# Optimization experiments

Hardware: AMD Instinct MI355X
Metric: run time of the kernel (lower is better)

## Reference

```python
import jax, jax.numpy as jnp
import numpy as np
from jax import lax

V, D, H, HR = 32000, 512, 1024, 2
T_SRC, T_TGT, T_REF, B, NREF = 128, 128, 32, 64, 4


def _gru_scan(x_emb, lengths, h0, Wih, Whh, bih, bhh):
    """Masked GRU over padded [T,B,D]; equivalent to torch pack->GRU->unpack.
    Returns (outputs [T,B,h] zeroed past lengths, final hidden [B,h])."""
    T = x_emb.shape[0]
    xW = jnp.einsum('tbd,gd->tbg', x_emb, Wih) + bih  # [T,B,3h] input-gate preacts

    def step(h, inp):
        xw, t = inp
        hw = h @ Whh.T + bhh
        xr, xz, xn = jnp.split(xw, 3, axis=-1)
        hr, hz, hn = jnp.split(hw, 3, axis=-1)
        r = jax.nn.sigmoid(xr + hr)
        z = jax.nn.sigmoid(xz + hz)
        n = jnp.tanh(xn + r * hn)
        h_new = (1.0 - z) * n + z * h
        m = (t < lengths)[:, None]
        h_next = jnp.where(m, h_new, h)   # freeze hidden past length (packing)
        out = jnp.where(m, h_new, 0.0)    # unpack pads with zeros
        return h_next, out

    hT, outs = lax.scan(step, h0, (xW, jnp.arange(T)))
    return outs, hT


def setup_inputs() -> dict:
    key = jax.random.key(0)
    ks = jax.random.split(key, 32)

    def u(k, shape, fan):
        lim = 1.0 / np.sqrt(fan)
        return jax.random.uniform(k, shape, jnp.float32, -lim, lim)

    inp = {}
    inp['tgt'] = jax.random.randint(ks[0], (T_TGT, B), 0, V)
    inp['tgt_lengths'] = jax.random.randint(ks[1], (B,), 1, T_TGT + 1)
    inp['src'] = jax.random.randint(ks[2], (T_SRC, B), 0, V)
    inp['src_lengths'] = jax.random.randint(ks[3], (B,), 1, T_SRC + 1)
    inp['ref_ids'] = jax.random.randint(ks[4], (NREF, T_REF, B), 0, V)
    inp['ref_lengths'] = jax.random.randint(ks[5], (NREF, B), 1, T_REF + 1)
    inp['emb'] = jax.random.normal(ks[6], (V, D), jnp.float32) * 0.02
    inp['src_Wih'] = u(ks[7], (3 * H, D), H)
    inp['src_Whh'] = u(ks[8], (3 * H, H), H)
    inp['src_bih'] = u(ks[9], (3 * H,), H)
    inp['src_bhh'] = u(ks[10], (3 * H,), H)
    inp['tgt_Wih'] = u(ks[11], (3 * H, D), H)
    inp['tgt_Whh'] = u(ks[12], (3 * H, H), H)
    inp['tgt_bih'] = u(ks[13], (3 * H,), H)
    inp['tgt_bhh'] = u(ks[14], (3 * H,), H)
    inp['ref_Wih'] = u(ks[15], (3 * HR, D), HR)
    inp['ref_Whh'] = u(ks[16], (3 * HR, HR), HR)
    inp['ref_bih'] = u(ks[17], (3 * HR,), HR)
    inp['ref_bhh'] = u(ks[18], (3 * HR,), HR)
    inp['p1_W'] = u(ks[19], (64, H), H)
    inp['p1_b'] = u(ks[20], (64,), H)
    inp['p2_W'] = u(ks[21], (2, 64), 64)
    inp['p2_b'] = u(ks[22], (2,), 64)
    return inp


def reference(tgt, tgt_lengths, src, src_lengths, ref_ids, ref_lengths, emb,
              src_Wih, src_Whh, src_bih, src_bhh,
              tgt_Wih, tgt_Whh, tgt_bih, tgt_bhh,
              ref_Wih, ref_Whh, ref_bih, ref_bhh,
              p1_W, p1_b, p2_W, p2_b):
    # --- src encoder ---
    src_emb = emb[src]  # [T_SRC,B,D]
    h0 = jnp.zeros((src.shape[1], src_Whh.shape[1]), emb.dtype)
    _, src_hT = _gru_scan(src_emb, src_lengths, h0, src_Wih, src_Whh, src_bih, src_bhh)

    # --- ref encoders: original loops in Python over the ref list with
    # per-ref sort/pack/tiny-GRU; here vectorized with vmap over NREF.
    # (Output is computed, as torch eager does, but does not feed logits.)
    ref_emb = emb[ref_ids]  # [NREF,T_REF,B,D]
    h0r = jnp.zeros((ref_ids.shape[2], ref_Whh.shape[1]), emb.dtype)
    ref_context, ref_hidden = jax.vmap(
        lambda e, l: _gru_scan(e, l, h0r, ref_Wih, ref_Whh, ref_bih, ref_bhh)
    )(ref_emb, ref_lengths)
    del ref_context, ref_hidden

    # --- tgt decoder initialized from src final hidden ---
    tgt_emb = emb[tgt]
    _, tgt_hT = _gru_scan(tgt_emb, tgt_lengths, src_hT, tgt_Wih, tgt_Whh, tgt_bih, tgt_bhh)

    # --- projection head (dropout = identity in eval) ---
    logits = jnp.tanh(tgt_hT @ p1_W.T + p1_b) @ p2_W.T + p2_b  # [B,2]
    return logits
```

## Files before the change

kernel.cpp:

```cpp
#include <hip/hip_runtime.h>
#include <stdint.h>

typedef short short8 __attribute__((ext_vector_type(8)));
typedef float f32x4 __attribute__((ext_vector_type(4)));
typedef float f32x2 __attribute__((ext_vector_type(2)));
typedef unsigned long long u64;

#define TSEQ   128
#define BATCH  64
#define DIM    512
#define HID    1024
#define G3     3072
#define MROWS  (TSEQ * BATCH)
#define NB     32
#define HB     32

__device__ __forceinline__ unsigned short f2bf(float f) {
  union { float f; unsigned u; } v; v.f = f;
  unsigned u = v.u;
  return (unsigned short)((u + 0x7FFFu + ((u >> 16) & 1u)) >> 16);
}

__device__ __forceinline__ short8 pack8(f32x4 a, f32x4 b) {
  short8 r;
  r[0] = (short)f2bf(a.x); r[1] = (short)f2bf(a.y);
  r[2] = (short)f2bf(a.z); r[3] = (short)f2bf(a.w);
  r[4] = (short)f2bf(b.x); r[5] = (short)f2bf(b.y);
  r[6] = (short)f2bf(b.z); r[7] = (short)f2bf(b.w);
  return r;
}

__device__ __forceinline__ u64 packbf4(float a, float b, float c, float d) {
  return (u64)f2bf(a) | ((u64)f2bf(b) << 16) | ((u64)f2bf(c) << 32) | ((u64)f2bf(d) << 48);
}

__device__ __forceinline__ float sigm(float x) { return 1.0f / (1.0f + __expf(-x)); }
__device__ __forceinline__ float tanh_fast(float x) { return 2.0f / (1.0f + __expf(-2.0f * x)) - 1.0f; }

__global__ __launch_bounds__(256) void prep_kernel(
    const int* __restrict__ ids, const float* __restrict__ emb,
    const float* __restrict__ wih, unsigned short* __restrict__ X,
    unsigned short* __restrict__ Wb, unsigned int* bars)
{
  int row = blockIdx.x;
  int tid = threadIdx.x;
  const float* srcp;
  unsigned short* dst;
  if (row < MROWS) {
    srcp = emb + (long)ids[row] * DIM;
    dst  = X + (long)row * DIM;
  } else {
    int wr = row - MROWS;
    srcp = wih + (long)wr * DIM;
    dst  = Wb + (long)wr * DIM;
  }
  int d = tid * 2;
  f32x2 v = *(const f32x2*)(srcp + d);
  unsigned pk = (unsigned)f2bf(v.x) | ((unsigned)f2bf(v.y) << 16);
  *(unsigned*)(dst + d) = pk;
  if (bars != nullptr && row == 0) ((f32x4*)bars)[tid] = (f32x4){};
}

#define BM 128
#define BN 128
#define BK 32

__global__ __launch_bounds__(256) void xw_gemm(
    const unsigned short* __restrict__ X,
    const unsigned short* __restrict__ W,
    const float* __restrict__ bih,
    float* __restrict__ out)
{
  __shared__ unsigned short As[BM * BK];
  __shared__ unsigned short Bs[BN * BK];
  int tid = threadIdx.x;
  int w = tid >> 6, l = tid & 63;
  int m0 = blockIdx.y * BM;
  int n0 = blockIdx.x * BN;
  int wr = w >> 1, wc = w & 1;

  int sr = tid >> 2, skq = tid & 3;
  int sr2 = sr + 64;
  int sgk  = (skq - (sr  >> 1)) & 3;
  int sgk2 = (skq - (sr2 >> 1)) & 3;
  const unsigned short* gA0 = X + (long)(m0 + sr ) * DIM + sgk  * 8;
  const unsigned short* gA1 = X + (long)(m0 + sr2) * DIM + sgk2 * 8;
  const unsigned short* gB0 = W + (long)(n0 + sr ) * DIM + sgk  * 8;
  const unsigned short* gB1 = W + (long)(n0 + sr2) * DIM + sgk2 * 8;
  unsigned short* lA0 = As + sr  * BK + skq * 8;
  unsigned short* lA1 = As + sr2 * BK + skq * 8;
  unsigned short* lB0 = Bs + sr  * BK + skq * 8;
  unsigned short* lB1 = Bs + sr2 * BK + skq * 8;

  f32x4 acc[4][4];
  #pragma unroll
  for (int mt = 0; mt < 4; ++mt)
    #pragma unroll
    for (int nt = 0; nt < 4; ++nt) acc[mt][nt] = (f32x4){};

  short8 va0 = *(const short8*)(gA0);
  short8 va1 = *(const short8*)(gA1);
  short8 vb0 = *(const short8*)(gB0);
  short8 vb1 = *(const short8*)(gB1);

  int fr = l & 15, fk = l >> 4;
  for (int kt = 0; kt < DIM / BK; ++kt) {
    __syncthreads();
    *(short8*)lA0 = va0; *(short8*)lA1 = va1;
    *(short8*)lB0 = vb0; *(short8*)lB1 = vb1;
    __syncthreads();
    if (kt + 1 < DIM / BK) {
      int ko = (kt + 1) * BK;
      va0 = *(const short8*)(gA0 + ko);
      va1 = *(const short8*)(gA1 + ko);
      vb0 = *(const short8*)(gB0 + ko);
      vb1 = *(const short8*)(gB1 + ko);
    }
    short8 af[4], bf[4];
    #pragma unroll
    for (int mt = 0; mt < 4; ++mt) {
      int r = wr * 64 + mt * 16 + fr;
      int slot = ((r >> 1) + fk) & 3;
      af[mt] = *(const short8*)(As + r * BK + slot * 8);
    }
    #pragma unroll
    for (int nt = 0; nt < 4; ++nt) {
      int r = wc * 64 + nt * 16 + fr;
      int slot = ((r >> 1) + fk) & 3;
      bf[nt] = *(const short8*)(Bs + r * BK + slot * 8);
    }
    #pragma unroll
    for (int mt = 0; mt < 4; ++mt)
      #pragma unroll
      for (int nt = 0; nt < 4; ++nt)
        acc[mt][nt] = __builtin_amdgcn_mfma_f32_16x16x32_bf16(af[mt], bf[nt], acc[mt][nt], 0, 0, 0);
  }

  #pragma unroll
  for (int nt = 0; nt < 4; ++nt) {
    int n = n0 + wc * 64 + nt * 16 + fr;
    float bias = bih[n];
    #pragma unroll
    for (int mt = 0; mt < 4; ++mt) {
      int mbase = m0 + wr * 64 + mt * 16 + fk * 4;
      #pragma unroll
      for (int r = 0; r < 4; ++r)
        out[(long)(mbase + r) * G3 + n] = acc[mt][nt][r] + bias;
    }
  }
}

#define MF(a, b, c) __builtin_amdgcn_mfma_f32_16x16x32_bf16(a, b, c, 0, 0, 0)

#define ISSUE(ss, kk) do { \
  asm volatile("global_load_dwordx4 %0, %1, off offset:%2 sc0" \
               : "=v"(bv[ss][0]) : "v"(ad0), "i"((kk) * 64) : "memory"); \
  asm volatile("global_load_dwordx4 %0, %1, off offset:%2 sc0" \
               : "=v"(bv[ss][1]) : "v"(ad1), "i"((kk) * 64) : "memory"); \
  asm volatile("global_load_dwordx4 %0, %1, off offset:%2 sc0" \
               : "=v"(bv[ss][2]) : "v"(ad2), "i"((kk) * 64) : "memory"); \
  asm volatile("global_load_dwordx4 %0, %1, off offset:%2 sc0" \
               : "=v"(bv[ss][3]) : "v"(ad3), "i"((kk) * 64) : "memory"); \
} while (0)

#define MF6(kk, ss, nt) \
  acc[0][nt] = MF(areg[0][kk], bv[ss][nt], acc[0][nt]); \
  acc[1][nt] = MF(areg[1][kk], bv[ss][nt], acc[1][nt]); \
  acc[2][nt] = MF(areg[2][kk], bv[ss][nt], acc[2][nt]); \
  acc[3][nt] = MF(areg[3][kk], bv[ss][nt], acc[3][nt]); \
  acc[4][nt] = MF(areg[4][kk], bv[ss][nt], acc[4][nt]); \
  acc[5][nt] = MF(areg[5][kk], bv[ss][nt], acc[5][nt]);

#define CONS(kk, ss, wn) do { \
  asm volatile("s_waitcnt vmcnt(" #wn ")" ::: "memory"); \
  __builtin_amdgcn_sched_barrier(0); \
  MF6(kk, ss, 0) MF6(kk, ss, 1) MF6(kk, ss, 2) MF6(kk, ss, 3) \
} while (0)

#define CONSI(kk, ss, wn, nk) do { CONS(kk, ss, wn); ISSUE(ss, nk); } while (0)

#define BARRIER_ARRIVE(tgtv) do { \
  asm volatile("s_waitcnt vmcnt(0)" ::: "memory"); \
  __syncthreads(); \
  if (tid == 0) { \
    unsigned fv_ = (unsigned)(tgtv); \
    uint64_t fa_ = (uint64_t)(bar + (blockIdx.x << 4)); \
    asm volatile("global_store_dword %0, %1, off sc0 sc1" :: "v"(fa_), "v"(fv_) : "memory"); \
  } \
} while (0)

#define BARRIER_WAIT(tgtv) do { \
  if (tid < NB) { \
    unsigned v_; \
    uint64_t pa_ = (uint64_t)(bar + (tid << 4)); \
    do { \
      asm volatile("global_load_dword %0, %1, off sc0 sc1" : "=v"(v_) : "v"(pa_) : "memory"); \
      asm volatile("s_waitcnt vmcnt(0)" ::: "memory"); \
    } while (__any(v_ < (unsigned)(tgtv))); \
  } \
  __syncthreads(); \
  asm volatile("buffer_inv sc1" ::: "memory"); \
} while (0)

__global__ __launch_bounds__(256, 1) void gru_kernel(
    const float* __restrict__ Whh, const float* __restrict__ bhh,
    const float* __restrict__ xw, const int* __restrict__ lengths,
    u64* __restrict__ hbf,
    float* __restrict__ hf32,
    unsigned int* __restrict__ bar, int T, int initzero)
{
  const int tid = threadIdx.x;
  const int w = tid >> 6, l = tid & 63;
  const int fr = l & 15, fk = l >> 4;
  const int U0 = blockIdx.x * HB;

  short8 areg[6][8];
  #pragma unroll
  for (int mt = 0; mt < 6; ++mt) {
    const int m = mt * 16 + fr;
    const int gate = m >> 5, u = m & 31;
    const float* wp = Whh + (size_t)(gate * HID + U0 + u) * HID + w * 256 + fk * 8;
    #pragma unroll
    for (int ksl = 0; ksl < 8; ++ksl) {
      f32x4 a0 = *(const f32x4*)(wp + ksl * 32);
      f32x4 a1 = *(const f32x4*)(wp + ksl * 32 + 4);
      areg[mt][ksl] = pack8(a0, a1);
    }
  }

  const int gb = l;
  const int j0 = w * 8;
  const size_t hoff = (size_t)gb * (HID / 4) + (size_t)(U0 + j0) / 4;
  const int len_b = lengths[gb];

  float h[8];
  #pragma unroll
  for (int j = 0; j < 8; ++j)
    h[j] = initzero ? 0.0f : hf32[(size_t)gb * HID + U0 + j0 + j];

  __shared__ float red2[4][64][100];
  __shared__ float bb[3][32];
  if (tid < 96) bb[tid >> 5][tid & 31] = bhh[(tid >> 5) * HID + U0 + (tid & 31)];

  f32x4 xrv[2], xzv[2], xnv[2];
  #define LOAD_XW(tt) do { \
    const float* xp_ = xw + ((size_t)(tt) * BATCH + gb) * G3 + U0 + j0; \
    xrv[0] = *(const f32x4*)(xp_);            xrv[1] = *(const f32x4*)(xp_ + 4); \
    xzv[0] = *(const f32x4*)(xp_ + HID);      xzv[1] = *(const f32x4*)(xp_ + HID + 4); \
    xnv[0] = *(const f32x4*)(xp_ + 2 * HID);  xnv[1] = *(const f32x4*)(xp_ + 2 * HID + 4); \
  } while (0)

  {
    union { u64 q[2]; f32x4 v4; } pk;
    pk.q[0] = packbf4(h[0], h[1], h[2], h[3]);
    pk.q[1] = packbf4(h[4], h[5], h[6], h[7]);
    uint64_t hw = (uint64_t)(hbf + hoff);
    asm volatile("global_store_dwordx4 %0, %1, off sc0 sc1" :: "v"(hw), "v"(pk.v4) : "memory");
    BARRIER_ARRIVE(1);
    LOAD_XW(0);
    BARRIER_WAIT(1);
  }

  for (int t = 0; t < T; ++t) {
    asm volatile("s_waitcnt vmcnt(0)" ::: "memory");

    const char* hbase = (const char*)hbf + (size_t)(t & 1) * (BATCH * (HID / 4) * 8);
    uint64_t ad0 = (uint64_t)(hbase + (size_t)(fr) * 2048 + w * 512 + fk * 16);
    uint64_t ad1 = ad0 + 16 * 2048;
    uint64_t ad2 = ad0 + 32 * 2048;
    uint64_t ad3 = ad0 + 48 * 2048;

    f32x4 acc[6][4];
    #pragma unroll
    for (int mt = 0; mt < 6; ++mt)
      #pragma unroll
      for (int nt = 0; nt < 4; ++nt) acc[mt][nt] = (f32x4){};

    short8 bv[6][4];
    ISSUE(0, 0); ISSUE(1, 1); ISSUE(2, 2); ISSUE(3, 3); ISSUE(4, 4); ISSUE(5, 5);
    CONSI(0, 0, 20, 6);
    CONSI(1, 1, 20, 7);
    CONS(2, 2, 20);
    CONS(3, 3, 16);
    CONS(4, 4, 12);
    CONS(5, 5, 8);
    CONS(6, 0, 4);
    CONS(7, 1, 0);

    #pragma unroll
    for (int mt = 0; mt < 6; ++mt)
      #pragma unroll
      for (int nt = 0; nt < 4; ++nt)
        *(f32x4*)&red2[w][nt * 16 + fr][mt * 16 + fk * 4] = acc[mt][nt];
    __syncthreads();

    #define RD4(s, row) (*(const f32x4*)&red2[s][gb][row])
    f32x4 sr_[2], sz_[2], sn_[2];
    #pragma unroll
    for (int hh = 0; hh < 2; ++hh) {
      const int rbase = j0 + hh * 4;
      sr_[hh] = RD4(0, rbase)      + RD4(1, rbase)      + RD4(2, rbase)      + RD4(3, rbase)      + *(const f32x4*)&bb[0][rbase];
      sz_[hh] = RD4(0, 32 + rbase) + RD4(1, 32 + rbase) + RD4(2, 32 + rbase) + RD4(3, 32 + rbase) + *(const f32x4*)&bb[1][rbase];
      sn_[hh] = RD4(0, 64 + rbase) + RD4(1, 64 + rbase) + RD4(2, 64 + rbase) + RD4(3, 64 + rbase) + *(const f32x4*)&bb[2][rbase];
    }

    const int upd = (t < len_b);
    #pragma unroll
    for (int j = 0; j < 8; ++j) {
      float rr = sigm(xrv[j >> 2][j & 3] + sr_[j >> 2][j & 3]);
      float zz = sigm(xzv[j >> 2][j & 3] + sz_[j >> 2][j & 3]);
      float nn = tanh_fast(xnv[j >> 2][j & 3] + rr * sn_[j >> 2][j & 3]);
      float cc = (1.0f - zz) * nn + zz * h[j];
      h[j] = upd ? cc : h[j];
    }

    if (t + 1 < T) {
      union { u64 q[2]; f32x4 v4; } pk;
      pk.q[0] = packbf4(h[0], h[1], h[2], h[3]);
      pk.q[1] = packbf4(h[4], h[5], h[6], h[7]);
      uint64_t hw = (uint64_t)((char*)hbf + (size_t)((t + 1) & 1) * (BATCH * (HID / 4) * 8) + hoff * 8);
      asm volatile("global_store_dwordx4 %0, %1, off sc0 sc1" :: "v"(hw), "v"(pk.v4) : "memory");
      BARRIER_ARRIVE(t + 2);
      LOAD_XW(t + 1);
      BARRIER_WAIT(t + 2);
    }
  }

  #pragma unroll
  for (int j = 0; j < 8; ++j)
    hf32[(size_t)gb * HID + U0 + j0 + j] = h[j];
}

__global__ __launch_bounds__(256) void head_kernel(
    const float* __restrict__ hf32, const float* __restrict__ p1W,
    const float* __restrict__ p1b, const float* __restrict__ p2W,
    const float* __restrict__ p2b, float* __restrict__ outp)
{
  int b = blockIdx.x;
  int tid = threadIdx.x;
  __shared__ float hrow[HID];
  __shared__ float red[4][64];
  __shared__ float s1[64];
  for (int d = tid; d < HID; d += 256) hrow[d] = hf32[(long)b * HID + d];
  __syncthreads();
  int j = tid & 63, q = tid >> 6;
  const float* wrow = p1W + (long)j * HID + q * 256;
  float s = 0.0f;
  for (int k = 0; k < 256; ++k) s += hrow[q * 256 + k] * wrow[k];
  red[q][j] = s;
  __syncthreads();
  if (tid < 64) {
    float v = red[0][tid] + red[1][tid] + red[2][tid] + red[3][tid] + p1b[tid];
    s1[tid] = tanh_fast(v);
  }
  __syncthreads();
  if (tid < 2) {
    float a = p2b[tid];
    for (int k = 0; k < 64; ++k) a += s1[k] * p2W[tid * 64 + k];
    outp[b * 2 + tid] = a;
  }
}

extern "C" void kernel_launch(void* const* d_in, const int* in_sizes, int n_in,
                              void* d_out, int out_size, void* d_ws, size_t ws_size,
                              hipStream_t stream) {
  const int*   tgt_ids = (const int*)d_in[0];
  const int*   tgt_len = (const int*)d_in[1];
  const int*   src_ids = (const int*)d_in[2];
  const int*   src_len = (const int*)d_in[3];
  const float* emb  = (const float*)d_in[6];
  const float* sWih = (const float*)d_in[7];
  const float* sWhh = (const float*)d_in[8];
  const float* sbih = (const float*)d_in[9];
  const float* sbhh = (const float*)d_in[10];
  const float* tWih = (const float*)d_in[11];
  const float* tWhh = (const float*)d_in[12];
  const float* tbih = (const float*)d_in[13];
  const float* tbhh = (const float*)d_in[14];
  const float* p1W  = (const float*)d_in[19];
  const float* p1b  = (const float*)d_in[20];
  const float* p2W  = (const float*)d_in[21];
  const float* p2b  = (const float*)d_in[22];

  char* ws = (char*)d_ws;
  size_t off = 0;
  float* xw = (float*)(ws + off);                   off += (size_t)MROWS * G3 * 4;
  unsigned short* X  = (unsigned short*)(ws + off); off += (size_t)MROWS * DIM * 2;
  unsigned short* Wb = (unsigned short*)(ws + off); off += (size_t)G3 * DIM * 2;
  u64* hbf = (u64*)(ws + off);                      off += 2ull * BATCH * (HID / 4) * 8;
  float* hf32 = (float*)(ws + off);                 off += (size_t)BATCH * HID * 4;
  unsigned int* bars = (unsigned int*)(ws + off);   off += 4096;
  if (ws_size < off) return;

  const int PREP_BLOCKS = MROWS + G3;

  prep_kernel<<<PREP_BLOCKS, 256, 0, stream>>>(src_ids, emb, sWih, X, Wb, bars);
  xw_gemm<<<dim3(G3 / BN, MROWS / BM), 256, 0, stream>>>(X, Wb, sbih, xw);
  gru_kernel<<<NB, 256, 0, stream>>>(sWhh, sbhh, xw, src_len, hbf, hf32, bars, TSEQ, 1);
  prep_kernel<<<PREP_BLOCKS, 256, 0, stream>>>(tgt_ids, emb, tWih, X, Wb, nullptr);
  xw_gemm<<<dim3(G3 / BN, MROWS / BM), 256, 0, stream>>>(X, Wb, tbih, xw);
  gru_kernel<<<NB, 256, 0, stream>>>(tWhh, tbhh, xw, tgt_len, hbf, hf32, bars + 512, TSEQ, 0);
  head_kernel<<<BATCH, 256, 0, stream>>>(hf32, p1W, p1b, p2W, p2b, (float*)d_out);
}
```

Baseline: 2.316 ms.

## Co-locate GRU blocks on a single XCC to use cheaper L2-scope barriers

The GRU kernel now launches 256 blocks. Each block reads its XCC id and claims a rank with an atomic counter. The first XCC to collect 32 blocks keeps them and the other blocks exit. A probe round checks that hidden-state stores with sc0-only visibility are seen by all 32 ranks; if so, the recurrent loop uses sc0-only stores and loads for hidden state and barrier flags and skips buffer_inv, which avoids cross-XCC coherence traffic on every timestep. This adds extra blocks, a startup handshake and a larger barrier workspace, and it relies on same-XCC L2 coherence; a fallback keeps the old scopes when the probe fails.

Measured after the change: 3.976 ms. 1.72x slower.

```diff
diff --git a/kernel.cpp b/kernel.cpp
--- a/kernel.cpp
+++ b/kernel.cpp
@@ -13,7 +13,13 @@
 #define G3     3072
 #define MROWS  (TSEQ * BATCH)
 #define NB     32
+#define GRID_GRU 256
 #define HB     32
+
+#define FLAGS_OFF 0
+#define PROBE_OFF 4096
+#define OK_OFF    8192
+#define CTL_OFF   12288
 
 __device__ __forceinline__ unsigned short f2bf(float f) {
   union { float f; unsigned u; } v; v.f = f;
@@ -58,7 +64,10 @@
   f32x2 v = *(const f32x2*)(srcp + d);
   unsigned pk = (unsigned)f2bf(v.x) | ((unsigned)f2bf(v.y) << 16);
   *(unsigned*)(dst + d) = pk;
-  if (bars != nullptr && row == 0) ((f32x4*)bars)[tid] = (f32x4){};
+  if (bars != nullptr && row == 0) {
+    #pragma unroll
+    for (int k = 0; k < 8; ++k) ((f32x4*)bars)[k * 256 + tid] = (f32x4){};
+  }
 }
 
 #define BM 128
@@ -179,86 +188,70 @@
 
 #define CONSI(kk, ss, wn, nk) do { CONS(kk, ss, wn); ISSUE(ss, nk); } while (0)
 
-#define BARRIER_ARRIVE(tgtv) do { \
-  asm volatile("s_waitcnt vmcnt(0)" ::: "memory"); \
-  __syncthreads(); \
-  if (tid == 0) { \
-    unsigned fv_ = (unsigned)(tgtv); \
-    uint64_t fa_ = (uint64_t)(bar + (blockIdx.x << 4)); \
-    asm volatile("global_store_dword %0, %1, off sc0 sc1" :: "v"(fa_), "v"(fv_) : "memory"); \
-  } \
-} while (0)
-
-#define BARRIER_WAIT(tgtv) do { \
-  if (tid < NB) { \
-    unsigned v_; \
-    uint64_t pa_ = (uint64_t)(bar + (tid << 4)); \
-    do { \
-      asm volatile("global_load_dword %0, %1, off sc0 sc1" : "=v"(v_) : "v"(pa_) : "memory"); \
-      asm volatile("s_waitcnt vmcnt(0)" ::: "memory"); \
-    } while (__any(v_ < (unsigned)(tgtv))); \
-  } \
-  __syncthreads(); \
-  asm volatile("buffer_inv sc1" ::: "memory"); \
-} while (0)
-
-__global__ __launch_bounds__(256, 1) void gru_kernel(
-    const float* __restrict__ Whh, const float* __restrict__ bhh,
-    const float* __restrict__ xw, const int* __restrict__ lengths,
-    u64* __restrict__ hbf,
-    float* __restrict__ hf32,
-    unsigned int* __restrict__ bar, int T, int initzero)
-{
-  const int tid = threadIdx.x;
-  const int w = tid >> 6, l = tid & 63;
-  const int fr = l & 15, fk = l >> 4;
-  const int U0 = blockIdx.x * HB;
-
-  short8 areg[6][8];
-  #pragma unroll
-  for (int mt = 0; mt < 6; ++mt) {
-    const int m = mt * 16 + fr;
-    const int gate = m >> 5, u = m & 31;
-    const float* wp = Whh + (size_t)(gate * HID + U0 + u) * HID + w * 256 + fk * 8;
-    #pragma unroll
-    for (int ksl = 0; ksl < 8; ++ksl) {
-      f32x4 a0 = *(const f32x4*)(wp + ksl * 32);
-      f32x4 a1 = *(const f32x4*)(wp + ksl * 32 + 4);
-      areg[mt][ksl] = pack8(a0, a1);
-    }
-  }
-
-  const int gb = l;
-  const int j0 = w * 8;
-  const size_t hoff = (size_t)gb * (HID / 4) + (size_t)(U0 + j0) / 4;
-  const int len_b = lengths[gb];
-
-  float h[8];
-  #pragma unroll
-  for (int j = 0; j < 8; ++j)
-    h[j] = initzero ? 0.0f : hf32[(size_t)gb * HID + U0 + j0 + j];
-
-  __shared__ float red2[4][64][100];
-  __shared__ float bb[3][32];
-  if (tid < 96) bb[tid >> 5][tid & 31] = bhh[(tid >> 5) * HID + U0 + (tid & 31)];
-
-  f32x4 xrv[2], xzv[2], xnv[2];
-  #define LOAD_XW(tt) do { \
+#define LOAD_XW(tt) do { \
     const float* xp_ = xw + ((size_t)(tt) * BATCH + gb) * G3 + U0 + j0; \
     xrv[0] = *(const f32x4*)(xp_);            xrv[1] = *(const f32x4*)(xp_ + 4); \
     xzv[0] = *(const f32x4*)(xp_ + HID);      xzv[1] = *(const f32x4*)(xp_ + HID + 4); \
     xnv[0] = *(const f32x4*)(xp_ + 2 * HID);  xnv[1] = *(const f32x4*)(xp_ + 2 * HID + 4); \
   } while (0)
 
+template<bool FAST>
+__device__ __forceinline__ void st_h16(uint64_t a, f32x4 v) {
+  if constexpr (FAST)
+    asm volatile("global_store_dwordx4 %0, %1, off sc0" :: "v"(a), "v"(v) : "memory");
+  else
+    asm volatile("global_store_dwordx4 %0, %1, off sc0 sc1" :: "v"(a), "v"(v) : "memory");
+}
+
+template<bool FAST>
+__device__ __forceinline__ void bar_arrive(unsigned* flags, unsigned rank, unsigned gen, int tid) {
+  asm volatile("s_waitcnt vmcnt(0)" ::: "memory");
+  __syncthreads();
+  if (tid == 0) {
+    uint64_t fa = (uint64_t)(flags + (rank << 4));
+    if constexpr (FAST)
+      asm volatile("global_store_dword %0, %1, off sc0" :: "v"(fa), "v"(gen) : "memory");
+    else
+      asm volatile("global_store_dword %0, %1, off sc0 sc1" :: "v"(fa), "v"(gen) : "memory");
+  }
+}
+
+template<bool FAST, bool INV>
+__device__ __forceinline__ void bar_wait(unsigned* flags, unsigned gen, int tid) {
+  if (tid < NB) {
+    unsigned v;
+    uint64_t pa = (uint64_t)(flags + (tid << 4));
+    do {
+      if constexpr (FAST)
+        asm volatile("global_load_dword %0, %1, off sc0" : "=v"(v) : "v"(pa) : "memory");
+      else
+        asm volatile("global_load_dword %0, %1, off sc0 sc1" : "=v"(v) : "v"(pa) : "memory");
+      asm volatile("s_waitcnt vmcnt(0)" ::: "memory");
+    } while (__any(v < gen));
+  }
+  __syncthreads();
+  if constexpr (INV) asm volatile("buffer_inv sc1" ::: "memory");
+}
+
+template<bool FAST>
+__device__ __forceinline__ void run_gru(
+    const short8 (&areg)[6][8], float (&h)[8],
+    const float* __restrict__ xw, u64* __restrict__ hbf,
+    unsigned* __restrict__ flags, float* __restrict__ hf32,
+    float (*red2)[64][100], float (*bb)[32],
+    int tid, int w, int fr, int fk, int gb, int j0,
+    unsigned rank, int U0, size_t hoff, int len_b, int T)
+{
+  f32x4 xrv[2], xzv[2], xnv[2];
+
   {
     union { u64 q[2]; f32x4 v4; } pk;
     pk.q[0] = packbf4(h[0], h[1], h[2], h[3]);
     pk.q[1] = packbf4(h[4], h[5], h[6], h[7]);
-    uint64_t hw = (uint64_t)(hbf + hoff);
-    asm volatile("global_store_dwordx4 %0, %1, off sc0 sc1" :: "v"(hw), "v"(pk.v4) : "memory");
-    BARRIER_ARRIVE(1);
+    st_h16<FAST>((uint64_t)(hbf + hoff), pk.v4);
+    bar_arrive<FAST>(flags, rank, 2u, tid);
     LOAD_XW(0);
-    BARRIER_WAIT(1);
+    bar_wait<FAST, !FAST>(flags, 2u, tid);
   }
 
   for (int t = 0; t < T; ++t) {
@@ -319,16 +312,119 @@
       pk.q[0] = packbf4(h[0], h[1], h[2], h[3]);
       pk.q[1] = packbf4(h[4], h[5], h[6], h[7]);
       uint64_t hw = (uint64_t)((char*)hbf + (size_t)((t + 1) & 1) * (BATCH * (HID / 4) * 8) + hoff * 8);
-      asm volatile("global_store_dwordx4 %0, %1, off sc0 sc1" :: "v"(hw), "v"(pk.v4) : "memory");
-      BARRIER_ARRIVE(t + 2);
+      st_h16<FAST>(hw, pk.v4);
+      bar_arrive<FAST>(flags, rank, (unsigned)(t + 3), tid);
       LOAD_XW(t + 1);
-      BARRIER_WAIT(t + 2);
+      bar_wait<FAST, !FAST>(flags, (unsigned)(t + 3), tid);
     }
   }
 
   #pragma unroll
   for (int j = 0; j < 8; ++j)
     hf32[(size_t)gb * HID + U0 + j0 + j] = h[j];
+}
+
+__global__ __launch_bounds__(256, 1) void gru_kernel(
+    const float* __restrict__ Whh, const float* __restrict__ bhh,
+    const float* __restrict__ xw, const int* __restrict__ lengths,
+    u64* __restrict__ hbf, float* __restrict__ hf32,
+    unsigned int* __restrict__ bar, int T, int initzero)
+{
+  const int tid = threadIdx.x;
+  const int w = tid >> 6, l = tid & 63;
+  const int fr = l & 15, fk = l >> 4;
+
+  unsigned* flags  = (unsigned*)((char*)bar + FLAGS_OFF);
+  unsigned* probes = (unsigned*)((char*)bar + PROBE_OFF);
+  unsigned* okf    = (unsigned*)((char*)bar + OK_OFF);
+  unsigned* ctl    = (unsigned*)((char*)bar + CTL_OFF);
+
+  __shared__ unsigned sh_rank, sh_ok, sh_fast;
+  if (tid == 0) {
+    sh_ok = 1u;
+    unsigned xcc;
+    asm volatile("s_getreg_b32 %0, hwreg(HW_REG_XCC_ID)" : "=s"(xcc));
+    xcc &= 7u;
+    unsigned r = __hip_atomic_fetch_add(&ctl[xcc], 1u, __ATOMIC_RELAXED, __HIP_MEMORY_SCOPE_AGENT);
+    if (r == (unsigned)NB - 1u) {
+      unsigned expected = 0u;
+      __hip_atomic_compare_exchange_strong(&ctl[8], &expected, xcc + 1u,
+          __ATOMIC_RELAXED, __ATOMIC_RELAXED, __HIP_MEMORY_SCOPE_AGENT);
+    }
+    unsigned c;
+    while ((c = __hip_atomic_load(&ctl[8], __ATOMIC_RELAXED, __HIP_MEMORY_SCOPE_AGENT)) == 0u)
+      __builtin_amdgcn_s_sleep(2);
+    sh_rank = (xcc == c - 1u && r < (unsigned)NB) ? r : 0xFFFFFFFFu;
+  }
+  __syncthreads();
+  const unsigned rank = sh_rank;
+  if (rank == 0xFFFFFFFFu) return;
+  const int U0 = (int)rank * HB;
+
+  if (tid == 0) {
+    unsigned pv = 0xC0DE0000u | rank;
+    uint64_t pa = (uint64_t)(probes + (rank << 4));
+    asm volatile("global_store_dword %0, %1, off sc0" :: "v"(pa), "v"(pv) : "memory");
+  }
+  bar_arrive<false>(flags, rank, 1u, tid);
+  bar_wait<false, false>(flags, 1u, tid);
+  if (tid < NB) {
+    unsigned v;
+    uint64_t pa = (uint64_t)(probes + (tid << 4));
+    asm volatile("global_load_dword %0, %1, off sc0" : "=v"(v) : "v"(pa) : "memory");
+    asm volatile("s_waitcnt vmcnt(0)" ::: "memory");
+    if (__any(v != (0xC0DE0000u | (unsigned)tid))) { if (tid == 0) sh_ok = 0u; }
+  }
+  __syncthreads();
+  if (tid == 0) {
+    unsigned ov = sh_ok + 1u;
+    uint64_t oa = (uint64_t)(okf + (rank << 4));
+    asm volatile("global_store_dword %0, %1, off sc0 sc1" :: "v"(oa), "v"(ov) : "memory");
+  }
+  if (tid < NB) {
+    unsigned v;
+    uint64_t oa = (uint64_t)(okf + (tid << 4));
+    do {
+      asm volatile("global_load_dword %0, %1, off sc0 sc1" : "=v"(v) : "v"(oa) : "memory");
+      asm volatile("s_waitcnt vmcnt(0)" ::: "memory");
+    } while (__any(v == 0u));
+    if (tid == 0) sh_fast = __all(v == 2u) ? 1u : 0u;
+  }
+  __syncthreads();
+  const bool fast = (sh_fast != 0u);
+
+  short8 areg[6][8];
+  #pragma unroll
+  for (int mt = 0; mt < 6; ++mt) {
+    const int m = mt * 16 + fr;
+    const int gate = m >> 5, u = m & 31;
+    const float* wp = Whh + (size_t)(gate * HID + U0 + u) * HID + w * 256 + fk * 8;
+    #pragma unroll
+    for (int ksl = 0; ksl < 8; ++ksl) {
+      f32x4 a0 = *(const f32x4*)(wp + ksl * 32);
+      f32x4 a1 = *(const f32x4*)(wp + ksl * 32 + 4);
+      areg[mt][ksl] = pack8(a0, a1);
+    }
+  }
+
+  const int gb = l;
+  const int j0 = w * 8;
+  const size_t hoff = (size_t)gb * (HID / 4) + (size_t)(U0 + j0) / 4;
+  const int len_b = lengths[gb];
+
+  float h[8];
+  #pragma unroll
+  for (int j = 0; j < 8; ++j)
+    h[j] = initzero ? 0.0f : hf32[(size_t)gb * HID + U0 + j0 + j];
+
+  __shared__ float red2[4][64][100];
+  __shared__ float bb[3][32];
+  if (tid < 96) bb[tid >> 5][tid & 31] = bhh[(tid >> 5) * HID + U0 + (tid & 31)];
+
+  if (fast)
+    run_gru<true >(areg, h, xw, hbf, flags, hf32, red2, bb, tid, w, fr, fk, gb, j0, rank, U0, hoff, len_b, T);
+  else
+    run_gru<false>(areg, h, xw, hbf, flags, hf32, red2, bb, tid, w, fr, fk, gb, j0, rank, U0, hoff, len_b, T);
 }
 
 __global__ __launch_bounds__(256) void head_kernel(
@@ -389,16 +485,16 @@
   unsigned short* Wb = (unsigned short*)(ws + off); off += (size_t)G3 * DIM * 2;
   u64* hbf = (u64*)(ws + off);                      off += 2ull * BATCH * (HID / 4) * 8;
   float* hf32 = (float*)(ws + off);                 off += (size_t)BATCH * HID * 4;
-  unsigned int* bars = (unsigned int*)(ws + off);   off += 4096;
+  unsigned int* bars = (unsigned int*)(ws + off);   off += 32768;
   if (ws_size < off) return;
 
   const int PREP_BLOCKS = MROWS + G3;
 
   prep_kernel<<<PREP_BLOCKS, 256, 0, stream>>>(src_ids, emb, sWih, X, Wb, bars);
   xw_gemm<<<dim3(G3 / BN, MROWS / BM), 256, 0, stream>>>(X, Wb, sbih, xw);
-  gru_kernel<<<NB, 256, 0, stream>>>(sWhh, sbhh, xw, src_len, hbf, hf32, bars, TSEQ, 1);
+  gru_kernel<<<GRID_GRU, 256, 0, stream>>>(sWhh, sbhh, xw, src_len, hbf, hf32, bars, TSEQ, 1);
   prep_kernel<<<PREP_BLOCKS, 256, 0, stream>>>(tgt_ids, emb, tWih, X, Wb, nullptr);
   xw_gemm<<<dim3(G3 / BN, MROWS / BM), 256, 0, stream>>>(X, Wb, tbih, xw);
-  gru_kernel<<<NB, 256, 0, stream>>>(tWhh, tbhh, xw, tgt_len, hbf, hf32, bars + 512, TSEQ, 0);
+  gru_kernel<<<GRID_GRU, 256, 0, stream>>>(tWhh, tbhh, xw, tgt_len, hbf, hf32, bars + 4096, TSEQ, 0);
   head_kernel<<<BATCH, 256, 0, stream>>>(hf32, p1W, p1b, p2W, p2b, (float*)d_out);
 }
```
